# Kernel optimization log

Hardware: AMD Instinct MI355X
Metric: run time of the kernel (lower is better)

## Reference

```python
import jax, jax.numpy as jnp
import numpy as np

B, S, D = 2, 2048, 2048
NQ, NKV, H = 16, 8, 256
G = NQ // NKV
SOFT_CAP = 50.0
WINDOW = 1024
MAX_WAVELENGTH = 10000.0


def _rope(x, start_index=0):
    # keras_hub RotaryEmbedding (rotate-half) followed by Gemma's interleave
    # reshape: stack(split(x,2,-1),axis=-1).reshape(shape). Net effect:
    # out[..., 2i] = x1*cos - x2*sin, out[..., 2i+1] = x2*cos + x1*sin.
    b, s, n, h = x.shape
    half = h // 2
    inv_freq = 1.0 / (MAX_WAVELENGTH ** (jnp.arange(0, h, 2, dtype=jnp.float32) / h))
    positions = start_index + jnp.arange(s, dtype=jnp.float32)
    freq = positions[:, None] * inv_freq[None, :]            # (s, h/2)
    cos = jnp.cos(freq)[None, :, None, :].astype(x.dtype)     # (1,s,1,h/2)
    sin = jnp.sin(freq)[None, :, None, :].astype(x.dtype)
    x1, x2 = x[..., :half], x[..., half:]
    r1 = x1 * cos - x2 * sin
    r2 = x2 * cos + x1 * sin
    return jnp.stack([r1, r2], axis=-1).reshape(b, s, n, h)


def setup_inputs() -> dict:
    key = jax.random.key(0)
    ks = jax.random.split(key, 5)
    x = jax.random.normal(ks[0], (B, S, D), dtype=jnp.float32)
    Wq = jax.random.normal(ks[1], (NQ, D, H), dtype=jnp.float32) * 0.02
    Wk = jax.random.normal(ks[2], (NKV, D, H), dtype=jnp.float32) * 0.02
    Wv = jax.random.normal(ks[3], (NKV, D, H), dtype=jnp.float32) * 0.02
    Wo = jax.random.normal(ks[4], (NQ, H, D), dtype=jnp.float32) * 0.02
    attention_mask = jnp.tril(jnp.ones((S, S), dtype=jnp.float32))  # causal
    return {"x": x, "Wq": Wq, "Wk": Wk, "Wv": Wv, "Wo": Wo,
            "attention_mask": attention_mask}


def reference(x, Wq, Wk, Wv, Wo, attention_mask):
    q = _rope(jnp.einsum('btd,ndh->btnh', x, Wq))   # (B,S,NQ,H)
    k = _rope(jnp.einsum('bsd,kdh->bskh', x, Wk))   # (B,S,NKV,H)
    v = jnp.einsum('bsd,kdh->bskh', x, Wv)          # (B,S,NKV,H)

    q = q * jnp.asarray(1.0 / np.sqrt(H), dtype=q.dtype)
    q = q.reshape(B, S, NKV, G, H)
    logits = jnp.einsum('btkgh,bskh->bkgts', q, k).astype(jnp.float32)

    # logit soft-cap
    logits = jnp.tanh(logits / SOFT_CAP) * SOFT_CAP

    # sliding-window band AND causal mask
    ones = jnp.ones((S, S), dtype=jnp.float32)
    sliding = jnp.triu(ones, -(WINDOW - 1)) * jnp.tril(ones, WINDOW - 1)
    mask = sliding * attention_mask                  # (S,S)

    # keras Softmax with mask: masked positions get -1e9 (fp32)
    masked = jnp.where(mask[None, None, None, :, :] > 0, logits,
                       jnp.float32(-1e9))
    probs = jax.nn.softmax(masked, axis=-1).astype(x.dtype)

    av = jnp.einsum('bkgts,bskh->btkgh', probs, v).reshape(B, S, NQ, H)

    # zero rows with no attended tokens (original causal mask)
    na = jnp.all(attention_mask == 0, axis=-1, keepdims=True)[..., None]  # (S,1,1)
    av = jnp.where(na, jnp.zeros_like(av), av)

    return jnp.einsum('btnh,nhd->btd', av, Wo)
```

## Files before the change

### kernel.cpp

```cpp
#include <hip/hip_runtime.h>
#include <stdint.h>

typedef __bf16 bf16_t;
typedef __bf16 bf16x8 __attribute__((ext_vector_type(8)));
typedef __bf16 bf16x4 __attribute__((ext_vector_type(4)));
typedef float f32x4 __attribute__((ext_vector_type(4)));

#define DEV static __device__ __forceinline__

#define SB 2
#define SS 2048
#define SD 2048
#define SNQ 16
#define SNKV 8
#define SH 256
#define SWIN 1024
#define QKVP 8192

DEV void async_ld16(const void* g, void* lds) {
  __builtin_amdgcn_global_load_lds(
      (const __attribute__((address_space(1))) void*)g,
      (__attribute__((address_space(3))) void*)lds, 16, 0, 0);
}

__global__ __launch_bounds__(256) void prep_kernel(
    const float* __restrict__ x, const float* __restrict__ Wq,
    const float* __restrict__ Wk, const float* __restrict__ Wv,
    const float* __restrict__ Wo, bf16_t* __restrict__ xb,
    bf16_t* __restrict__ wqkvT, bf16_t* __restrict__ woT) {
  __shared__ bf16_t T[64 * 72];
  int bid = blockIdx.x;
  if (bid < 8192) {
    const int i = bid * 256 + threadIdx.x;
    float4 v = ((const float4*)x)[i];
    bf16x4 o = {(bf16_t)v.x, (bf16_t)v.y, (bf16_t)v.z, (bf16_t)v.w};
    *(bf16x4*)(xb + (size_t)i * 4) = o;
    return;
  }
  bid -= 8192;
  const float* ip;
  bf16_t* op;
  int R, C, r0, c0;
  if (bid < 4096) {
    const int zg = bid >> 7, rest = bid & 127;
    r0 = (rest >> 2) * 64;
    c0 = (rest & 3) * 64;
    ip = (zg < 16) ? (Wq + (size_t)zg * SD * SH)
       : (zg < 24) ? (Wk + (size_t)(zg - 16) * SD * SH)
                   : (Wv + (size_t)(zg - 24) * SD * SH);
    op = wqkvT + (size_t)zg * SD * SH;
    R = SD; C = SH;
  } else {
    bid -= 4096;
    r0 = (bid >> 5) * 64;
    c0 = (bid & 31) * 64;
    ip = Wo; op = woT; R = SNQ * SH; C = SD;
  }
  const int tc = threadIdx.x & 15;
  const int tr = threadIdx.x >> 4;
#pragma unroll
  for (int i = 0; i < 4; ++i) {
    const int r = tr + i * 16;
    float4 v = *(const float4*)(ip + (size_t)(r0 + r) * C + c0 + tc * 4);
    float vv[4] = {v.x, v.y, v.z, v.w};
#pragma unroll
    for (int e = 0; e < 4; ++e) {
      const int row = tc * 4 + e;
      *(bf16_t*)((char*)T + row * 144 + ((r * 2) ^ (((row >> 3) & 7) << 4))) =
          (bf16_t)vv[e];
    }
  }
  __syncthreads();
  const int tc2 = threadIdx.x & 7, tr2 = threadIdx.x >> 3;
#pragma unroll
  for (int i = 0; i < 2; ++i) {
    const int row = tr2 + i * 32;
    bf16x8 v = *(const bf16x8*)((const char*)T + row * 144 +
                                ((tc2 * 16) ^ (((row >> 3) & 7) << 4)));
    *(bf16x8*)(op + (size_t)(c0 + row) * R + r0 + tc2 * 8) = v;
  }
}

template <int BN, int MODE>
__global__ __launch_bounds__(512, 1) void gemm8p(const bf16_t* __restrict__ A,
                                                 const bf16_t* __restrict__ Bt,
                                                 void* __restrict__ Cout,
                                                 bf16_t* __restrict__ kbp,
                                                 bf16_t* __restrict__ vtp,
                                                 int M, int N, int K) {
  constexpr int WM = (BN == 256) ? 2 : 4;
  constexpr int WN = 8 / WM;
  constexpr int MQ = 4 / WM;
  constexpr int BH = BN / 128;
  constexpr int SMEM = 65536 + BH * 32768;
  __shared__ char smem[SMEM];
  bf16_t* AsBase = (bf16_t*)smem;
  bf16_t* BsBase = (bf16_t*)(smem + 65536);

  const int tid = threadIdx.x, lane = tid & 63, wid = tid >> 6;
  const int xcd = blockIdx.x & 7, ii = blockIdx.x >> 3;
  int by, bx;
  if (BN == 256) { by = (xcd & 1) * 8 + (ii >> 3); bx = (xcd >> 1) * 8 + (ii & 7); }
  else           { by = (xcd & 3) * 4 + (ii >> 3); bx = (xcd >> 2) * 8 + (ii & 7); }
  const int row0 = by << 8, col0 = bx * BN;
  const int wr = wid / WN, wc = wid % WN;
  const int lr = lane & 15, hi = lane >> 4;

  const bf16_t* Arow = A + (size_t)row0 * K;
  const bf16_t* Brow = Bt + (size_t)col0 * K;

  auto stageHA = [&](int t, int h) {
#pragma unroll
    for (int i = 0; i < 2; ++i) {
      const int f = tid + (i << 9);
      const int r = (h << 7) + (f >> 3), pc = f & 7;
      async_ld16(Arow + (size_t)r * K + (t << 6) + (pc ^ (r & 7)) * 8,
                 (char*)(AsBase + (t & 1) * (256 * 64)) + (h << 14) + f * 16);
    }
  };
  auto stageHB = [&](int t, int h) {
#pragma unroll
    for (int i = 0; i < 2; ++i) {
      const int f = tid + (i << 9);
      const int r = (h << 7) + (f >> 3), pc = f & 7;
      async_ld16(Brow + (size_t)r * K + (t << 6) + (pc ^ (r & 7)) * 8,
                 (char*)(BsBase + (t & 1) * (BN * 64)) + (h << 14) + f * 16);
    }
  };

  f32x4 acc[4 * MQ][4];
#pragma unroll
  for (int m = 0; m < 4 * MQ; ++m)
#pragma unroll
    for (int n = 0; n < 4; ++n) acc[m][n] = f32x4{0.f, 0.f, 0.f, 0.f};

  const int NT = K >> 6;
  stageHB(0, 0);
  if (BH == 2) stageHB(0, 1);
  stageHA(0, 0); stageHA(0, 1);
  asm volatile("s_waitcnt vmcnt(2)" ::: "memory");
  __builtin_amdgcn_s_barrier();
  __builtin_amdgcn_sched_barrier(0);

  for (int t = 0; t < NT; ++t) {
    const bool pre = (t + 1 < NT);
    const char* Ab = (const char*)(AsBase + (t & 1) * (256 * 64));
    const char* Bb = (const char*)(BsBase + (t & 1) * (BN * 64));
    bf16x8 bfr[4][2];

#pragma unroll
    for (int q = 0; q < 4; ++q) {
      if (q == 0) {
#pragma unroll
        for (int nf = 0; nf < 4; ++nf)
#pragma unroll
          for (int ks = 0; ks < 2; ++ks) {
            const int r = nf * (16 * WN) + wc * 16 + lr;
            bfr[nf][ks] = *(const bf16x8*)(Bb + r * 128 +
                                           ((((ks << 2) + hi) ^ (r & 7)) << 4));
          }
      }
      bf16x8 af[MQ][2];
#pragma unroll
      for (int mq = 0; mq < MQ; ++mq)
#pragma unroll
        for (int ks = 0; ks < 2; ++ks) {
          const int r = q * 64 + mq * (16 * WM) + wr * 16 + lr;
          af[mq][ks] = *(const bf16x8*)(Ab + r * 128 +
                                        ((((ks << 2) + hi) ^ (r & 7)) << 4));
        }
      if (pre) {
        if (BH == 2) {
          if (q == 0) stageHB(t + 1, 0);
          if (q == 1) stageHB(t + 1, 1);
          if (q == 2) stageHA(t + 1, 0);
          if (q == 3) stageHA(t + 1, 1);
        } else {
          if (q == 0) stageHB(t + 1, 0);
          if (q == 1) stageHA(t + 1, 0);
          if (q == 2) stageHA(t + 1, 1);
        }
      }
      __builtin_amdgcn_s_setprio(1);
#pragma unroll
      for (int mq = 0; mq < MQ; ++mq)
#pragma unroll
        for (int nf = 0; nf < 4; ++nf)
#pragma unroll
          for (int ks = 0; ks < 2; ++ks)
            acc[q * MQ + mq][nf] = __builtin_amdgcn_mfma_f32_16x16x32_bf16(
                af[mq][ks], bfr[nf][ks], acc[q * MQ + mq][nf], 0, 0, 0);
      __builtin_amdgcn_s_setprio(0);
      if (q == 1) {
        if (pre) asm volatile("s_waitcnt vmcnt(4)" ::: "memory");
        else     asm volatile("s_waitcnt vmcnt(0)" ::: "memory");
        __builtin_amdgcn_s_barrier();
        __builtin_amdgcn_sched_barrier(0);
      }
      if (q == 3 && pre) {
        asm volatile("s_waitcnt vmcnt(2)" ::: "memory");
        __builtin_amdgcn_s_barrier();
        __builtin_amdgcn_sched_barrier(0);
      }
    }
  }

  if (MODE == 1 && bx >= 16 && bx < 24) {
    const int kv = bx - 16;
#pragma unroll
    for (int mf = 0; mf < 4 * MQ; ++mf) {
      const int r = row0 + (mf / MQ) * 64 + (mf % MQ) * (16 * WM) + wr * 16 + hi * 4;
#pragma unroll
      for (int nfp = 0; nfp < 2; ++nfp) {
        const int h = nfp * 64 + wc * 16 + lr;
        const float inv = __expf((float)h * -0.07195578f);
#pragma unroll
        for (int j = 0; j < 4; ++j) {
          const int rg = r + j;
          const int tpos = rg & (SS - 1), b = rg >> 11;
          const float fr = (float)tpos * inv;
          const float cs = __cosf(fr), sn = __sinf(fr);
          const float x1 = acc[mf][nfp][j], x2 = acc[mf][nfp + 2][j];
          bf16_t* kp = kbp + ((size_t)(b * SNKV + kv) * SS + tpos) * SH + h;
          kp[0] = (bf16_t)(x1 * cs - x2 * sn);
          kp[128] = (bf16_t)(x2 * cs + x1 * sn);
        }
      }
    }
  } else if (MODE == 1 && bx >= 24) {
    bf16_t* T = (bf16_t*)smem;
    __syncthreads();
    const int kv = bx - 24;
#pragma unroll
    for (int mf = 0; mf < 4 * MQ; ++mf) {
      const int tl = (mf / MQ) * 64 + (mf % MQ) * (16 * WM) + wr * 16 + hi * 4;
#pragma unroll
      for (int nf = 0; nf < 4; ++nf) {
        const int h = nf * (16 * WN) + wc * 16 + lr;
        bf16x4 v4 = {(bf16_t)acc[mf][nf][0], (bf16_t)acc[mf][nf][1],
                     (bf16_t)acc[mf][nf][2], (bf16_t)acc[mf][nf][3]};
        *(bf16x4*)((char*)T + h * 512 + ((tl * 2) ^ ((h & 7) << 4))) = v4;
      }
    }
    __syncthreads();
    const int b = row0 >> 11, t0b = row0 & (SS - 1);
    bf16_t* vbase = vtp + (size_t)(b * SNKV + kv) * SH * SS;
#pragma unroll
    for (int it = 0; it < 16; ++it) {
      const int f = tid + (it << 9);
      const int h = f >> 5, sl = f & 31;
      bf16x8 v = *(const bf16x8*)((const char*)T + h * 512 +
                                  ((sl << 4) ^ ((h & 7) << 4)));
      *(bf16x8*)(vbase + (size_t)h * SS + t0b + sl * 8) = v;
    }
  } else {
#pragma unroll
    for (int mf = 0; mf < 4 * MQ; ++mf) {
      const int r = row0 + (mf / MQ) * 64 + (mf % MQ) * (16 * WM) + wr * 16 + hi * 4;
#pragma unroll
      for (int nf = 0; nf < 4; ++nf) {
        const int c = col0 + nf * (16 * WN) + wc * 16 + lr;
#pragma unroll
        for (int j = 0; j < 4; ++j) {
          if (MODE == 2)
            ((float*)Cout)[(size_t)(r + j) * N + c] = acc[mf][nf][j];
          else
            ((bf16_t*)Cout)[(size_t)(r + j) * N + c] = (bf16_t)acc[mf][nf][j];
        }
      }
    }
  }
}

#define QB 128
#define KVB 64
#define PP 72

__global__ __launch_bounds__(512, 2) void attn_kernel(
    const bf16_t* __restrict__ Q,
    const bf16_t* __restrict__ Kt,
    const bf16_t* __restrict__ Vt,
    bf16_t* __restrict__ AV) {
  __shared__ bf16_t Ks[2][KVB * SH];
  __shared__ bf16_t Vs[2][SH * KVB];
  __shared__ bf16_t Ps[QB * PP];

  const int tid = threadIdx.x, lane = tid & 63, wid = tid >> 6;
  const int x = blockIdx.x & 7;
  const int y = blockIdx.x >> 3;
  const int qt = 15 - (y & 15);
  const int head = (x << 1) | ((y >> 4) & 1);
  const int b = y >> 5;
  const int kvh = x;
  const int t0 = qt << 7;
  const int trw = t0 + wid * 16;
  const int lr = lane & 15, hi = lane >> 4;
  const int lk = hi << 3;
  const int lq = hi;

  bf16x8 qf[8];
  {
    const bf16_t* qp = Q + ((size_t)(b * SS + trw + lr)) * QKVP + head * SH + lk;
#pragma unroll
    for (int ks = 0; ks < 8; ++ks) qf[ks] = *(const bf16x8*)(qp + ks * 32);
    const float tpos = (float)(trw + lr);
#pragma unroll
    for (int ks = 0; ks < 4; ++ks) {
      bf16x8 a = qf[ks], b2 = qf[ks + 4];
      bf16x8 ra, rb;
#pragma unroll
      for (int e = 0; e < 8; ++e) {
        float c_ = (float)(ks * 32 + lk + e);
        float inv = __expf(c_ * -0.07195578f);
        float fr = tpos * inv;
        float cs = __cosf(fr), sn = __sinf(fr);
        float x1 = (float)a[e], x2 = (float)b2[e];
        ra[e] = (bf16_t)((x1 * cs - x2 * sn) * 0.0625f);
        rb[e] = (bf16_t)((x2 * cs + x1 * sn) * 0.0625f);
      }
      qf[ks] = ra; qf[ks + 4] = rb;
    }
  }

  f32x4 o[16];
#pragma unroll
  for (int i = 0; i < 16; ++i) o[i] = f32x4{0.f, 0.f, 0.f, 0.f};
  float lsum[4] = {0.f, 0.f, 0.f, 0.f};

  const bf16_t* Kb = Kt + (size_t)(b * SNKV + kvh) * SS * SH;
  const bf16_t* Vb = Vt + (size_t)(b * SNKV + kvh) * SH * SS;

  const int sv0 = (t0 >= SWIN) ? ((t0 >> 6) - 16) : 0;
  const int sv1 = (t0 >> 6) + 1;

  auto stage = [&](int s0, int d) {
#pragma unroll
    for (int it = 0; it < 4; ++it) {
      const int f = tid + (it << 9);
      {
        const int r = f >> 5, pc = f & 31;
        const int sc = pc ^ (r & 7);
        async_ld16(Kb + (size_t)(s0 + r) * SH + sc * 8, (char*)Ks[d] + f * 16);
      }
      {
        const int r = f >> 3, pc = f & 7;
        const int sc = pc ^ (r & 7);
        async_ld16(Vb + (size_t)r * SS + s0 + sc * 8, (char*)Vs[d] + f * 16);
      }
    }
  };

  stage(sv0 << 6, 0);
  __syncthreads();

  int cur = 0;
  for (int sv = sv0; sv <= sv1; ++sv, cur ^= 1) {
    if (sv < sv1) stage((sv + 1) << 6, cur ^ 1);

    const int s0 = sv << 6;
    const bool skip = (s0 > trw + 15) || (s0 + 63 < trw - (SWIN - 1));
    if (!skip) {
      const bf16_t* Kc = Ks[cur];
      const bf16_t* Vc = Vs[cur];
      f32x4 sacc[4];
#pragma unroll
      for (int nt = 0; nt < 4; ++nt) sacc[nt] = f32x4{0.f, 0.f, 0.f, 0.f};
      __builtin_amdgcn_s_setprio(1);
#pragma unroll
      for (int ks = 0; ks < 8; ++ks) {
#pragma unroll
        for (int nt = 0; nt < 4; ++nt) {
          const int R = nt * 16 + lr;
          bf16x8 kf = *(const bf16x8*)((const char*)Kc + R * 512 +
                                       (((ks * 4 + hi) ^ (R & 7)) << 4));
          sacc[nt] = __builtin_amdgcn_mfma_f32_16x16x32_bf16(qf[ks], kf, sacc[nt], 0, 0, 0);
        }
      }
      __builtin_amdgcn_s_setprio(0);

      const bool full = (s0 + 63 <= trw) && (s0 >= trw + 15 - (SWIN - 1));
      if (full) {
#pragma unroll
        for (int nt = 0; nt < 4; ++nt) {
#pragma unroll
          for (int j = 0; j < 4; ++j) {
            float u = sacc[nt][j] * 0.04f;
            float th = 50.f - 100.f * __builtin_amdgcn_rcpf(__expf(u) + 1.f);
            float p = __expf(th);
            lsum[j] += p;
            Ps[(wid * 16 + lq * 4 + j) * PP + nt * 16 + lr] = (bf16_t)p;
          }
        }
      } else {
#pragma unroll
        for (int nt = 0; nt < 4; ++nt) {
          const int s_ = s0 + nt * 16 + lr;
#pragma unroll
          for (int j = 0; j < 4; ++j) {
            const int t_ = trw + lq * 4 + j;
            float u = sacc[nt][j] * 0.04f;
            float th = 50.f - 100.f * __builtin_amdgcn_rcpf(__expf(u) + 1.f);
            const bool valid = (s_ <= t_) && (t_ - s_ < SWIN);
            float p = valid ? __expf(th) : 0.f;
            lsum[j] += p;
            Ps[(wid * 16 + lq * 4 + j) * PP + nt * 16 + lr] = (bf16_t)p;
          }
        }
      }

      __builtin_amdgcn_s_setprio(1);
#pragma unroll
      for (int ks = 0; ks < 2; ++ks) {
        bf16x8 pf = *(const bf16x8*)&Ps[(wid * 16 + lr) * PP + ks * 32 + lk];
#pragma unroll
        for (int nt = 0; nt < 16; ++nt) {
          const int R = nt * 16 + lr;
          bf16x8 vf = *(const bf16x8*)((const char*)Vc + R * 128 +
                                       (((ks * 4 + hi) ^ (R & 7)) << 4));
          o[nt] = __builtin_amdgcn_mfma_f32_16x16x32_bf16(pf, vf, o[nt], 0, 0, 0);
        }
      }
      __builtin_amdgcn_s_setprio(0);
    }

    __syncthreads();
  }

#pragma unroll
  for (int j = 0; j < 4; ++j) {
    float l = lsum[j];
    l += __shfl_xor(l, 1);
    l += __shfl_xor(l, 2);
    l += __shfl_xor(l, 4);
    l += __shfl_xor(l, 8);
    const float inv = 1.f / l;
    const int t_ = trw + lq * 4 + j;
    bf16_t* op = AV + ((size_t)(b * SS + t_)) * (SNQ * SH) + head * SH;
#pragma unroll
    for (int nt = 0; nt < 16; ++nt) op[nt * 16 + lr] = (bf16_t)(o[nt][j] * inv);
  }
}

extern "C" void kernel_launch(void* const* d_in, const int* in_sizes, int n_in,
                              void* d_out, int out_size, void* d_ws, size_t ws_size,
                              hipStream_t stream) {
  const float* x = (const float*)d_in[0];
  const float* Wq = (const float*)d_in[1];
  const float* Wk = (const float*)d_in[2];
  const float* Wv = (const float*)d_in[3];
  const float* Wo = (const float*)d_in[4];
  float* out = (float*)d_out;

  char* ws = (char*)d_ws;
  size_t off = 0;
  auto alloc = [&](size_t elems) {
    bf16_t* p = (bf16_t*)(ws + off);
    off += ((elems * 2 + 255) & ~(size_t)255);
    return p;
  };
  const size_t MS = (size_t)SB * SS;
  bf16_t* xb     = alloc(MS * SD);
  bf16_t* wqkvT  = alloc((size_t)QKVP * SD);
  bf16_t* woT    = alloc((size_t)SD * SNQ * SH);
  bf16_t* qkv    = alloc(MS * QKVP);
  bf16_t* kb     = alloc(MS * SNKV * SH);
  bf16_t* vt     = alloc(MS * SNKV * SH);
  bf16_t* av     = alloc(MS * SNQ * SH);
  (void)ws_size;

  prep_kernel<<<14336, 256, 0, stream>>>(x, Wq, Wk, Wv, Wo, xb, wqkvT, woT);

  gemm8p<256, 1><<<512, 512, 0, stream>>>(xb, wqkvT, qkv, kb, vt, 4096, QKVP, 2048);

  attn_kernel<<<512, 512, 0, stream>>>(qkv, kb, vt, av);

  gemm8p<128, 2><<<256, 512, 0, stream>>>(av, woT, out, nullptr, nullptr, 4096, 2048, 4096);
}
```

Baseline: 322.4 us.

## Split QK^T into column pairs interleaved with softcap-exp and relax launch bounds

Measured after the change: 328.8 us. No clear change (+2.0%).

```diff
diff --git a/kernel.cpp b/kernel.cpp
--- a/kernel.cpp
+++ b/kernel.cpp
@@ -276,7 +276,7 @@
 #define KVB 64
 #define PP 72
 
-__global__ __launch_bounds__(512, 2) void attn_kernel(
+__global__ __launch_bounds__(512, 1) void attn_kernel(
     const bf16_t* __restrict__ Q,
     const bf16_t* __restrict__ Kt,
     const bf16_t* __restrict__ Vt,
@@ -362,46 +362,42 @@
     if (!skip) {
       const bf16_t* Kc = Ks[cur];
       const bf16_t* Vc = Vs[cur];
-      f32x4 sacc[4];
-#pragma unroll
-      for (int nt = 0; nt < 4; ++nt) sacc[nt] = f32x4{0.f, 0.f, 0.f, 0.f};
-      __builtin_amdgcn_s_setprio(1);
-#pragma unroll
-      for (int ks = 0; ks < 8; ++ks) {
-#pragma unroll
-        for (int nt = 0; nt < 4; ++nt) {
-          const int R = nt * 16 + lr;
-          bf16x8 kf = *(const bf16x8*)((const char*)Kc + R * 512 +
-                                       (((ks * 4 + hi) ^ (R & 7)) << 4));
-          sacc[nt] = __builtin_amdgcn_mfma_f32_16x16x32_bf16(qf[ks], kf, sacc[nt], 0, 0, 0);
-        }
-      }
-      __builtin_amdgcn_s_setprio(0);
-
       const bool full = (s0 + 63 <= trw) && (s0 >= trw + 15 - (SWIN - 1));
-      if (full) {
-#pragma unroll
-        for (int nt = 0; nt < 4; ++nt) {
+
+#pragma unroll
+      for (int np = 0; np < 2; ++np) {
+        f32x4 sa0 = f32x4{0.f, 0.f, 0.f, 0.f};
+        f32x4 sa1 = f32x4{0.f, 0.f, 0.f, 0.f};
+        const int R0 = (np * 2) * 16 + lr;
+        const int R1 = (np * 2 + 1) * 16 + lr;
+        __builtin_amdgcn_s_setprio(1);
+#pragma unroll
+        for (int ks = 0; ks < 8; ++ks) {
+          bf16x8 kf0 = *(const bf16x8*)((const char*)Kc + R0 * 512 +
+                                        (((ks * 4 + hi) ^ (R0 & 7)) << 4));
+          bf16x8 kf1 = *(const bf16x8*)((const char*)Kc + R1 * 512 +
+                                        (((ks * 4 + hi) ^ (R1 & 7)) << 4));
+          sa0 = __builtin_amdgcn_mfma_f32_16x16x32_bf16(qf[ks], kf0, sa0, 0, 0, 0);
+          sa1 = __builtin_amdgcn_mfma_f32_16x16x32_bf16(qf[ks], kf1, sa1, 0, 0, 0);
+        }
+        __builtin_amdgcn_s_setprio(0);
+#pragma unroll
+        for (int half = 0; half < 2; ++half) {
+          const f32x4 sa = half ? sa1 : sa0;
+          const int nt = np * 2 + half;
 #pragma unroll
           for (int j = 0; j < 4; ++j) {
-            float u = sacc[nt][j] * 0.04f;
+            float u = sa[j] * 0.04f;
             float th = 50.f - 100.f * __builtin_amdgcn_rcpf(__expf(u) + 1.f);
-            float p = __expf(th);
-            lsum[j] += p;
-            Ps[(wid * 16 + lq * 4 + j) * PP + nt * 16 + lr] = (bf16_t)p;
-          }
-        }
-      } else {
-#pragma unroll
-        for (int nt = 0; nt < 4; ++nt) {
-          const int s_ = s0 + nt * 16 + lr;
-#pragma unroll
-          for (int j = 0; j < 4; ++j) {
-            const int t_ = trw + lq * 4 + j;
-            float u = sacc[nt][j] * 0.04f;
-            float th = 50.f - 100.f * __builtin_amdgcn_rcpf(__expf(u) + 1.f);
-            const bool valid = (s_ <= t_) && (t_ - s_ < SWIN);
-            float p = valid ? __expf(th) : 0.f;
+            float p;
+            if (full) {
+              p = __expf(th);
+            } else {
+              const int s_ = s0 + nt * 16 + lr;
+              const int t_ = trw + lq * 4 + j;
+              const bool valid = (s_ <= t_) && (t_ - s_ < SWIN);
+              p = valid ? __expf(th) : 0.f;
+            }
             lsum[j] += p;
             Ps[(wid * 16 + lq * 4 + j) * PP + nt * 16 + lr] = (bf16_t)p;
           }
```
